# Kernel optimization log

Hardware: AMD Instinct MI355X
Metric: run time of the kernel (lower is better)

The kernel has to match this reference:

```python
import jax, jax.numpy as jnp
import numpy as np

QMAX = 127.0
EPS = 1e-08


def setup_inputs() -> dict:
    key = jax.random.key(0)
    k1, k2, k3 = jax.random.split(key, 3)
    x = jax.random.normal(k1, (4, 2048, 4096), dtype=jnp.float32)
    weight = jax.random.normal(k2, (4096, 4096), dtype=jnp.float32) * 0.02
    bias = jax.random.normal(k3, (4096,), dtype=jnp.float32) * 0.02
    return {"x": x, "weight": weight, "bias": bias}


def _quantize_weight_per_row(weight):
    # Int8WeightLinear._q_per_row: per-output-row symmetric absmax scales,
    # scale stored as fp16 (then used as fp32 at runtime).
    w = weight.astype(jnp.float32)
    s = jnp.maximum(jnp.max(jnp.abs(w), axis=1, keepdims=True), EPS) / QMAX  # [out,1]
    q = jnp.clip(jnp.round(w / s), -QMAX, QMAX).astype(jnp.int8)             # [out,in]
    s = s[:, 0].astype(jnp.float16).astype(jnp.float32)                      # [out]
    return q, s


def _quantize_activation_per_row(x2d):
    # _quantize_activation_int8_2d: per-token absmax via max(amax, -amin).
    absmax = jnp.maximum(jnp.max(x2d, axis=1), -jnp.min(x2d, axis=1))
    sc = jnp.maximum(absmax.astype(jnp.float32), EPS) / QMAX                  # [rows]
    q = jnp.clip(jnp.round(x2d.astype(jnp.float32) / sc[:, None]), -QMAX, QMAX).astype(jnp.int8)
    return q, sc


def reference(x, weight, bias):
    w_q, w_s = _quantize_weight_per_row(weight)          # int8 [out,in], fp32 [out]
    x2d = x.reshape(-1, x.shape[-1])                      # [rows, in]
    xq, x_sc = _quantize_activation_per_row(x2d)          # int8 [rows,in], fp32 [rows]
    y = jnp.matmul(xq, w_q.T, preferred_element_type=jnp.int32).astype(jnp.float32)
    y = y * x_sc[:, None] * w_s[None, :]                  # [rows, out]
    out = y.astype(x.dtype).reshape(*x.shape[:-1], weight.shape[0])
    # bias buffer is stored fp16 and cast back to activation dtype
    out = out + bias.astype(jnp.float16).astype(x.dtype)
    return out
```

## Files before the change

### kernel.cpp

```cpp
#include <hip/hip_runtime.h>
#include <hip/hip_fp16.h>

typedef int v4i __attribute__((ext_vector_type(4)));

#define QMAXF 127.0f
#define EPSF 1e-8f

template <bool WEIGHT>
__global__ __launch_bounds__(256) void quant_rows(
    const float* __restrict__ src, signed char* __restrict__ q,
    float* __restrict__ scale, int ncols) {
  const int row = blockIdx.x;
  const int t = threadIdx.x;
  const float4* s4 = (const float4*)(src + (size_t)row * ncols);

  float4 v[4];
  float am = 0.f;
#pragma unroll
  for (int p = 0; p < 4; ++p) {
    v[p] = s4[p * 256 + t];
    am = fmaxf(am, fmaxf(fmaxf(fabsf(v[p].x), fabsf(v[p].y)),
                         fmaxf(fabsf(v[p].z), fabsf(v[p].w))));
  }
#pragma unroll
  for (int off = 32; off > 0; off >>= 1) am = fmaxf(am, __shfl_xor(am, off));
  __shared__ float red[4];
  if ((t & 63) == 0) red[t >> 6] = am;
  __syncthreads();
  am = fmaxf(fmaxf(red[0], red[1]), fmaxf(red[2], red[3]));

  const float s = fmaxf(am, EPSF) / QMAXF;

  uint32_t* qrow = (uint32_t*)(q + (size_t)row * ncols);
#pragma unroll
  for (int p = 0; p < 4; ++p) {
    float fx = fminf(fmaxf(rintf(v[p].x / s), -QMAXF), QMAXF);
    float fy = fminf(fmaxf(rintf(v[p].y / s), -QMAXF), QMAXF);
    float fz = fminf(fmaxf(rintf(v[p].z / s), -QMAXF), QMAXF);
    float fw = fminf(fmaxf(rintf(v[p].w / s), -QMAXF), QMAXF);
    uint32_t packed = ((uint32_t)((int)fx & 0xff)) |
                      ((uint32_t)((int)fy & 0xff) << 8) |
                      ((uint32_t)((int)fz & 0xff) << 16) |
                      ((uint32_t)((int)fw & 0xff) << 24);
    qrow[p * 256 + t] = packed;
  }
  if (t == 0) {
    float so = s;
    if (WEIGHT) so = __half2float(__float2half(s));
    scale[row] = so;
  }
}

__device__ __forceinline__ void gload16(const void* g, void* l) {
  __builtin_amdgcn_global_load_lds(
      (const __attribute__((address_space(1))) void*)g,
      (__attribute__((address_space(3))) void*)l, 16, 0, 0);
}

#define STAGE_A(dst, br0, ktoff)                                            \
  do {                                                                      \
    gload16(Ap + (size_t)((br0) + lr) * K + (ktoff) + scsw,                 \
            (dst) + ((br0) + lr) * 128 + sc);                               \
    gload16(Ap + (size_t)((br0) + 128 + lr) * K + (ktoff) + scsw,           \
            (dst) + ((br0) + 128 + lr) * 128 + sc);                         \
  } while (0)

#define STAGE_B(dst, nh, ktoff)                                             \
  do {                                                                      \
    const int r_ = (nh)*32 + lr + (lr & 32);                                \
    gload16(Bp + (size_t)(r_) * K + (ktoff) + scsw, (dst) + r_ * 128 + sc); \
    gload16(Bp + (size_t)(r_ + 128) * K + (ktoff) + scsw,                   \
            (dst) + (r_ + 128) * 128 + sc);                                 \
  } while (0)

#define READ_AF(MH)                                                         \
  _Pragma("unroll") for (int mi = 0; mi < 4; ++mi)                          \
      _Pragma("unroll") for (int ks = 0; ks < 2; ++ks)                      \
          af[mi][ks] = *(const v4i*)(Ad + (arow + ((MH)*4 + mi) * 16) *     \
                                              128 +                        \
                                     ((ac0 + ks * 64) ^ axor))

#define READ_BF(dst, NH)                                                    \
  _Pragma("unroll") for (int ni = 0; ni < 2; ++ni)                          \
      _Pragma("unroll") for (int ks = 0; ks < 2; ++ks)                      \
          dst[ni][ks] = *(const v4i*)(Bd + (brow + ((NH)*2 + ni) * 16) *    \
                                               128 +                       \
                                      ((ac0 + ks * 64) ^ bxor))

#define MFMA_QUAD(MH, NH, BFREG)                                            \
  _Pragma("unroll") for (int ks = 0; ks < 2; ++ks)                          \
      _Pragma("unroll") for (int mi = 0; mi < 4; ++mi)                      \
          _Pragma("unroll") for (int ni = 0; ni < 2; ++ni)                  \
              acc[(MH)*4 + mi][(NH)*2 + ni] =                               \
                  __builtin_amdgcn_mfma_i32_16x16x64_i8(                    \
                      af[mi][ks], BFREG[ni][ks],                            \
                      acc[(MH)*4 + mi][(NH)*2 + ni], 0, 0, 0)

__global__ __launch_bounds__(512, 2) void gemm_i8(
    const signed char* __restrict__ A,
    const signed char* __restrict__ B,
    const float* __restrict__ xsc,
    const float* __restrict__ wsc,
    const float* __restrict__ bias,
    float* __restrict__ out, int M, int N, int K) {
  __shared__ __align__(16) signed char lds[131072];
  signed char* const ldsA = lds;
  signed char* const ldsB = lds + 65536;

  const int tid = threadIdx.x;
  const int lane = tid & 63;
  const int wid = tid >> 6;
  const int wm = wid >> 2;
  const int wn = wid & 3;
  const int bm0 = blockIdx.x * 256;
  const int bn0 = blockIdx.y * 256;

  const signed char* Ap = A + (size_t)bm0 * K;
  const signed char* Bp = B + (size_t)bn0 * K;

  const int lr = tid >> 3;
  const int sc = (tid & 7) << 4;
  const int scsw = sc ^ ((lr & 7) << 4);

  const int arow = wm * 128 + (lane & 15);
  const int brow = wn * 64 + (lane & 15);
  const int ac0 = (lane >> 4) << 4;
  const int axor = (arow & 7) << 4;
  const int bxor = (brow & 7) << 4;

  v4i acc[8][4];
#pragma unroll
  for (int i = 0; i < 8; ++i)
#pragma unroll
    for (int j = 0; j < 4; ++j) acc[i][j] = (v4i){0, 0, 0, 0};

  const int NKT = K >> 7;

  STAGE_A(ldsA, 0, 0);
  STAGE_B(ldsB, 0, 0);
  STAGE_A(ldsA, 64, 0);
  STAGE_B(ldsB, 1, 0);
  STAGE_A(ldsA + 32768, 0, 128);
  STAGE_B(ldsB + 32768, 0, 128);
  asm volatile("s_waitcnt vmcnt(4)" ::: "memory");
  __builtin_amdgcn_sched_barrier(0);
  __builtin_amdgcn_s_barrier();

  for (int kt = 0; kt < NKT; ++kt) {
    const int d = kt & 1;
    const signed char* Ad = ldsA + d * 32768;
    const signed char* Bd = ldsB + d * 32768;
    signed char* const An = ldsA + (d ^ 1) * 32768;
    signed char* const Bn = ldsB + (d ^ 1) * 32768;
    const int ko1 = (kt + 1) << 7;
    const int ko2 = (kt + 2) << 7;

    v4i af[4][2];
    v4i bf0[2][2];
    v4i bf1[2][2];

    READ_AF(0);
    READ_BF(bf0, 0);
    READ_BF(bf1, 1);
    if (kt + 1 < NKT) {
      STAGE_A(An, 64, ko1);
      STAGE_B(Bn, 1, ko1);
    }
    __builtin_amdgcn_s_setprio(1);
    MFMA_QUAD(0, 0, bf0);
    MFMA_QUAD(0, 1, bf1);
    __builtin_amdgcn_s_setprio(0);
    __builtin_amdgcn_s_barrier();

    READ_AF(1);
    if (kt + 2 < NKT) {
      STAGE_A((signed char*)Ad, 0, ko2);
      STAGE_B((signed char*)Bd, 0, ko2);
    }
    __builtin_amdgcn_s_setprio(1);
    MFMA_QUAD(1, 0, bf0);
    MFMA_QUAD(1, 1, bf1);
    __builtin_amdgcn_s_setprio(0);
    if (kt < NKT - 2) {
      asm volatile("s_waitcnt vmcnt(4)" ::: "memory");
    } else {
      asm volatile("s_waitcnt vmcnt(0)" ::: "memory");
    }
    __builtin_amdgcn_sched_barrier(0);
    __builtin_amdgcn_s_barrier();
  }

#pragma unroll
  for (int mi = 0; mi < 8; ++mi) {
    const int m0 = bm0 + wm * 128 + mi * 16 + ((lane >> 4) << 2);
    const float4 xs = *(const float4*)&xsc[m0];
    const float xsv[4] = {xs.x, xs.y, xs.z, xs.w};
#pragma unroll
    for (int ni = 0; ni < 4; ++ni) {
      const int n = bn0 + wn * 64 + ni * 16 + (lane & 15);
      const float wsn = wsc[n];
      const float bn_ = __half2float(__float2half(bias[n]));
#pragma unroll
      for (int r = 0; r < 4; ++r) {
        out[(size_t)(m0 + r) * N + n] =
            (float)acc[mi][ni][r] * xsv[r] * wsn + bn_;
      }
    }
  }
}

extern "C" void kernel_launch(void* const* d_in, const int* in_sizes, int n_in,
                              void* d_out, int out_size, void* d_ws,
                              size_t ws_size, hipStream_t stream) {
  const float* x = (const float*)d_in[0];
  const float* w = (const float*)d_in[1];
  const float* bias = (const float*)d_in[2];
  float* out = (float*)d_out;

  const int K = 4096;
  const int Nw = in_sizes[1] / K;
  const int M = in_sizes[0] / K;

  signed char* wq = (signed char*)d_ws;
  signed char* xq = wq + (size_t)Nw * K;
  float* wsc = (float*)(xq + (size_t)M * K);
  float* xsc = wsc + Nw;

  quant_rows<true><<<Nw, 256, 0, stream>>>(w, wq, wsc, K);
  quant_rows<false><<<M, 256, 0, stream>>>(x, xq, xsc, K);

  dim3 g2(M / 256, Nw / 256, 1);
  gemm_i8<<<g2, 512, 0, stream>>>(xq, wq, xsc, wsc, bias, out, M, Nw, K);
}
```

Before: 178.5 us.

## Simplify GEMM pipeline to one barrier per k-tile with k-slice MFMA ordering

Replaces the split half-tile prefetch schedule, which used two barriers per iteration and a partial vmcnt wait, with a plain double buffer. The whole next tile is staged at the top of each iteration and fully awaited at the end. The MFMA loop now iterates by k-slice (all 8x4 tiles per 64-wide slice) instead of by M/N quadrant, cutting one barrier per tile. The cost is less overlap between global loads and compute and higher register pressure from holding 8 A fragments and two sets of 4 B fragments at once.

```diff
diff --git a/kernel.cpp b/kernel.cpp
--- a/kernel.cpp
+++ b/kernel.cpp
@@ -38,11 +38,10 @@
     float fy = fminf(fmaxf(rintf(v[p].y / s), -QMAXF), QMAXF);
     float fz = fminf(fmaxf(rintf(v[p].z / s), -QMAXF), QMAXF);
     float fw = fminf(fmaxf(rintf(v[p].w / s), -QMAXF), QMAXF);
-    uint32_t packed = ((uint32_t)((int)fx & 0xff)) |
-                      ((uint32_t)((int)fy & 0xff) << 8) |
-                      ((uint32_t)((int)fz & 0xff) << 16) |
-                      ((uint32_t)((int)fw & 0xff) << 24);
-    qrow[p * 256 + t] = packed;
+    qrow[p * 256 + t] = ((uint32_t)((int)fx & 0xff)) |
+                        ((uint32_t)((int)fy & 0xff) << 8) |
+                        ((uint32_t)((int)fz & 0xff) << 16) |
+                        ((uint32_t)((int)fw & 0xff) << 24);
   }
   if (t == 0) {
     float so = s;
@@ -73,28 +72,21 @@
             (dst) + (r_ + 128) * 128 + sc);                                 \
   } while (0)
 
-#define READ_AF(MH)                                                         \
-  _Pragma("unroll") for (int mi = 0; mi < 4; ++mi)                          \
-      _Pragma("unroll") for (int ks = 0; ks < 2; ++ks)                      \
-          af[mi][ks] = *(const v4i*)(Ad + (arow + ((MH)*4 + mi) * 16) *     \
-                                              128 +                        \
-                                     ((ac0 + ks * 64) ^ axor))
-
-#define READ_BF(dst, NH)                                                    \
-  _Pragma("unroll") for (int ni = 0; ni < 2; ++ni)                          \
-      _Pragma("unroll") for (int ks = 0; ks < 2; ++ks)                      \
-          dst[ni][ks] = *(const v4i*)(Bd + (brow + ((NH)*2 + ni) * 16) *    \
-                                               128 +                       \
-                                      ((ac0 + ks * 64) ^ bxor))
-
-#define MFMA_QUAD(MH, NH, BFREG)                                            \
-  _Pragma("unroll") for (int ks = 0; ks < 2; ++ks)                          \
-      _Pragma("unroll") for (int mi = 0; mi < 4; ++mi)                      \
-          _Pragma("unroll") for (int ni = 0; ni < 2; ++ni)                  \
-              acc[(MH)*4 + mi][(NH)*2 + ni] =                               \
-                  __builtin_amdgcn_mfma_i32_16x16x64_i8(                    \
-                      af[mi][ks], BFREG[ni][ks],                            \
-                      acc[(MH)*4 + mi][(NH)*2 + ni], 0, 0, 0)
+#define READ_AF64(ks)                                                       \
+  _Pragma("unroll") for (int mi = 0; mi < 8; ++mi)                          \
+      af[mi] = *(const v4i*)(Ad + (arow + mi * 16) * 128 +                  \
+                             ((ac0 + (ks)*64) ^ axor))
+
+#define READ_BF64(dst, ks)                                                  \
+  _Pragma("unroll") for (int ni = 0; ni < 4; ++ni)                          \
+      dst[ni] = *(const v4i*)(Bd + (brow + ni * 16) * 128 +                 \
+                              ((ac0 + (ks)*64) ^ bxor))
+
+#define MFMA_SET(AF, BF)                                                    \
+  _Pragma("unroll") for (int mi = 0; mi < 8; ++mi)                          \
+      _Pragma("unroll") for (int ni = 0; ni < 4; ++ni)                      \
+          acc[mi][ni] = __builtin_amdgcn_mfma_i32_16x16x64_i8(              \
+              AF[mi], BF[ni], acc[mi][ni], 0, 0, 0)
 
 __global__ __launch_bounds__(512, 2) void gemm_i8(
     const signed char* __restrict__ A,
@@ -137,12 +129,10 @@
   const int NKT = K >> 7;
 
   STAGE_A(ldsA, 0, 0);
+  STAGE_A(ldsA, 64, 0);
   STAGE_B(ldsB, 0, 0);
-  STAGE_A(ldsA, 64, 0);
   STAGE_B(ldsB, 1, 0);
-  STAGE_A(ldsA + 32768, 0, 128);
-  STAGE_B(ldsB + 32768, 0, 128);
-  asm volatile("s_waitcnt vmcnt(4)" ::: "memory");
+  asm volatile("s_waitcnt vmcnt(0)" ::: "memory");
   __builtin_amdgcn_sched_barrier(0);
   __builtin_amdgcn_s_barrier();
 
@@ -153,39 +143,28 @@
     signed char* const An = ldsA + (d ^ 1) * 32768;
     signed char* const Bn = ldsB + (d ^ 1) * 32768;
     const int ko1 = (kt + 1) << 7;
-    const int ko2 = (kt + 2) << 7;
-
-    v4i af[4][2];
-    v4i bf0[2][2];
-    v4i bf1[2][2];
-
-    READ_AF(0);
-    READ_BF(bf0, 0);
-    READ_BF(bf1, 1);
+
+    v4i af[8];
+    v4i bf[4];
+    v4i bf2[4];
+
     if (kt + 1 < NKT) {
+      STAGE_A(An, 0, ko1);
       STAGE_A(An, 64, ko1);
+      STAGE_B(Bn, 0, ko1);
       STAGE_B(Bn, 1, ko1);
     }
+    READ_BF64(bf, 0);
+    READ_AF64(0);
+    READ_BF64(bf2, 1);
     __builtin_amdgcn_s_setprio(1);
-    MFMA_QUAD(0, 0, bf0);
-    MFMA_QUAD(0, 1, bf1);
+    MFMA_SET(af, bf);
     __builtin_amdgcn_s_setprio(0);
-    __builtin_amdgcn_s_barrier();
-
-    READ_AF(1);
-    if (kt + 2 < NKT) {
-      STAGE_A((signed char*)Ad, 0, ko2);
-      STAGE_B((signed char*)Bd, 0, ko2);
-    }
+    READ_AF64(1);
     __builtin_amdgcn_s_setprio(1);
-    MFMA_QUAD(1, 0, bf0);
-    MFMA_QUAD(1, 1, bf1);
+    MFMA_SET(af, bf2);
     __builtin_amdgcn_s_setprio(0);
-    if (kt < NKT - 2) {
-      asm volatile("s_waitcnt vmcnt(4)" ::: "memory");
-    } else {
-      asm volatile("s_waitcnt vmcnt(0)" ::: "memory");
-    }
+    asm volatile("s_waitcnt vmcnt(0)" ::: "memory");
     __builtin_amdgcn_sched_barrier(0);
     __builtin_amdgcn_s_barrier();
   }
```

New measurement: 184.8 us. 3.5% more time.

## Use 16 waves per GEMM block and merge quantization kernels

Applied to the files above, without the earlier changes.

The int8 GEMM block grows from 512 to 1024 threads over the same 256x256 tile, so each wave now owns a 64x64 sub-tile with half the accumulators, and each thread issues one async LDS load per stage instead of two. Wait counts are adjusted to match. The weight and activation quantization passes are merged into one launch to save a kernel launch. More waves can hide latency better, but launch_bounds(1024,4) cannot fit with 128KB of LDS per block and the register budget per thread becomes tight. More waves per tile also means more LDS fragment reads per MFMA.

```diff
diff --git a/kernel.cpp b/kernel.cpp
--- a/kernel.cpp
+++ b/kernel.cpp
@@ -6,11 +6,17 @@
 #define QMAXF 127.0f
 #define EPSF 1e-8f
 
-template <bool WEIGHT>
-__global__ __launch_bounds__(256) void quant_rows(
-    const float* __restrict__ src, signed char* __restrict__ q,
-    float* __restrict__ scale, int ncols) {
-  const int row = blockIdx.x;
+__global__ __launch_bounds__(256) void quant_all(
+    const float* __restrict__ w, const float* __restrict__ x,
+    signed char* __restrict__ wq, signed char* __restrict__ xq,
+    float* __restrict__ wsc, float* __restrict__ xsc, int Nw, int ncols) {
+  const int b = blockIdx.x;
+  const bool is_w = b < Nw;
+  const int row = is_w ? b : b - Nw;
+  const float* __restrict__ src = is_w ? w : x;
+  signed char* __restrict__ q = is_w ? wq : xq;
+  float* __restrict__ scale = is_w ? wsc : xsc;
+
   const int t = threadIdx.x;
   const float4* s4 = (const float4*)(src + (size_t)row * ncols);
 
@@ -38,17 +44,12 @@
     float fy = fminf(fmaxf(rintf(v[p].y / s), -QMAXF), QMAXF);
     float fz = fminf(fmaxf(rintf(v[p].z / s), -QMAXF), QMAXF);
     float fw = fminf(fmaxf(rintf(v[p].w / s), -QMAXF), QMAXF);
-    uint32_t packed = ((uint32_t)((int)fx & 0xff)) |
-                      ((uint32_t)((int)fy & 0xff) << 8) |
-                      ((uint32_t)((int)fz & 0xff) << 16) |
-                      ((uint32_t)((int)fw & 0xff) << 24);
-    qrow[p * 256 + t] = packed;
-  }
-  if (t == 0) {
-    float so = s;
-    if (WEIGHT) so = __half2float(__float2half(s));
-    scale[row] = so;
-  }
+    qrow[p * 256 + t] = ((uint32_t)((int)fx & 0xff)) |
+                        ((uint32_t)((int)fy & 0xff) << 8) |
+                        ((uint32_t)((int)fz & 0xff) << 16) |
+                        ((uint32_t)((int)fw & 0xff) << 24);
+  }
+  if (t == 0) scale[row] = is_w ? __half2float(__float2half(s)) : s;
 }
 
 __device__ __forceinline__ void gload16(const void* g, void* l) {
@@ -59,44 +60,38 @@
 
 #define STAGE_A(dst, br0, ktoff)                                            \
   do {                                                                      \
-    gload16(Ap + (size_t)((br0) + lr) * K + (ktoff) + scsw,                 \
-            (dst) + ((br0) + lr) * 128 + sc);                               \
-    gload16(Ap + (size_t)((br0) + 128 + lr) * K + (ktoff) + scsw,           \
-            (dst) + ((br0) + 128 + lr) * 128 + sc);                         \
+    const int ar_ = (br0) + (lr & 63) + ((lr >> 6) << 7);                   \
+    gload16(Ap + (size_t)ar_ * K + (ktoff) + scsw,                          \
+            (dst) + ar_ * 128 + sc);                                        \
   } while (0)
 
 #define STAGE_B(dst, nh, ktoff)                                             \
   do {                                                                      \
-    const int r_ = (nh)*32 + lr + (lr & 32);                                \
-    gload16(Bp + (size_t)(r_) * K + (ktoff) + scsw, (dst) + r_ * 128 + sc); \
-    gload16(Bp + (size_t)(r_ + 128) * K + (ktoff) + scsw,                   \
-            (dst) + (r_ + 128) * 128 + sc);                                 \
+    const int br_ = (nh)*32 + (lr & 31) + ((lr >> 5) << 6);                 \
+    gload16(Bp + (size_t)br_ * K + (ktoff) + scsw,                          \
+            (dst) + br_ * 128 + sc);                                        \
   } while (0)
 
-#define READ_AF(MH)                                                         \
-  _Pragma("unroll") for (int mi = 0; mi < 4; ++mi)                          \
+#define READ_AF(AF, MB)                                                     \
+  _Pragma("unroll") for (int mi = 0; mi < 2; ++mi)                          \
       _Pragma("unroll") for (int ks = 0; ks < 2; ++ks)                      \
-          af[mi][ks] = *(const v4i*)(Ad + (arow + ((MH)*4 + mi) * 16) *     \
-                                              128 +                        \
+          AF[mi][ks] = *(const v4i*)(Ad + (arow + ((MB) + mi) * 16) * 128 + \
                                      ((ac0 + ks * 64) ^ axor))
 
-#define READ_BF(dst, NH)                                                    \
-  _Pragma("unroll") for (int ni = 0; ni < 2; ++ni)                          \
+#define READ_BF_ALL()                                                       \
+  _Pragma("unroll") for (int ni = 0; ni < 4; ++ni)                          \
       _Pragma("unroll") for (int ks = 0; ks < 2; ++ks)                      \
-          dst[ni][ks] = *(const v4i*)(Bd + (brow + ((NH)*2 + ni) * 16) *    \
-                                               128 +                       \
-                                      ((ac0 + ks * 64) ^ bxor))
-
-#define MFMA_QUAD(MH, NH, BFREG)                                            \
+          bf[ni][ks] = *(const v4i*)(Bd + (brow + ni * 16) * 128 +          \
+                                     ((ac0 + ks * 64) ^ bxor))
+
+#define MFMA_HALF(MB, AF)                                                   \
   _Pragma("unroll") for (int ks = 0; ks < 2; ++ks)                          \
-      _Pragma("unroll") for (int mi = 0; mi < 4; ++mi)                      \
-          _Pragma("unroll") for (int ni = 0; ni < 2; ++ni)                  \
-              acc[(MH)*4 + mi][(NH)*2 + ni] =                               \
-                  __builtin_amdgcn_mfma_i32_16x16x64_i8(                    \
-                      af[mi][ks], BFREG[ni][ks],                            \
-                      acc[(MH)*4 + mi][(NH)*2 + ni], 0, 0, 0)
-
-__global__ __launch_bounds__(512, 2) void gemm_i8(
+      _Pragma("unroll") for (int mi = 0; mi < 2; ++mi)                      \
+          _Pragma("unroll") for (int ni = 0; ni < 4; ++ni)                  \
+              acc[(MB) + mi][ni] = __builtin_amdgcn_mfma_i32_16x16x64_i8(   \
+                  AF[mi][ks], bf[ni][ks], acc[(MB) + mi][ni], 0, 0, 0)
+
+__global__ __launch_bounds__(1024, 4) void gemm_i8(
     const signed char* __restrict__ A,
     const signed char* __restrict__ B,
     const float* __restrict__ xsc,
@@ -122,15 +117,15 @@
   const int sc = (tid & 7) << 4;
   const int scsw = sc ^ ((lr & 7) << 4);
 
-  const int arow = wm * 128 + (lane & 15);
+  const int arow = wm * 64 + (lane & 15);
   const int brow = wn * 64 + (lane & 15);
   const int ac0 = (lane >> 4) << 4;
   const int axor = (arow & 7) << 4;
   const int bxor = (brow & 7) << 4;
 
-  v4i acc[8][4];
-#pragma unroll
-  for (int i = 0; i < 8; ++i)
+  v4i acc[4][4];
+#pragma unroll
+  for (int i = 0; i < 4; ++i)
 #pragma unroll
     for (int j = 0; j < 4; ++j) acc[i][j] = (v4i){0, 0, 0, 0};
 
@@ -142,7 +137,7 @@
   STAGE_B(ldsB, 1, 0);
   STAGE_A(ldsA + 32768, 0, 128);
   STAGE_B(ldsB + 32768, 0, 128);
-  asm volatile("s_waitcnt vmcnt(4)" ::: "memory");
+  asm volatile("s_waitcnt vmcnt(2)" ::: "memory");
   __builtin_amdgcn_sched_barrier(0);
   __builtin_amdgcn_s_barrier();
 
@@ -155,34 +150,30 @@
     const int ko1 = (kt + 1) << 7;
     const int ko2 = (kt + 2) << 7;
 
-    v4i af[4][2];
-    v4i bf0[2][2];
-    v4i bf1[2][2];
-
-    READ_AF(0);
-    READ_BF(bf0, 0);
-    READ_BF(bf1, 1);
+    v4i af[2][2];
+    v4i bf[4][2];
+
+    READ_AF(af, 0);
+    READ_BF_ALL();
     if (kt + 1 < NKT) {
       STAGE_A(An, 64, ko1);
       STAGE_B(Bn, 1, ko1);
     }
     __builtin_amdgcn_s_setprio(1);
-    MFMA_QUAD(0, 0, bf0);
-    MFMA_QUAD(0, 1, bf1);
+    MFMA_HALF(0, af);
     __builtin_amdgcn_s_setprio(0);
     __builtin_amdgcn_s_barrier();
 
-    READ_AF(1);
+    READ_AF(af, 2);
     if (kt + 2 < NKT) {
       STAGE_A((signed char*)Ad, 0, ko2);
       STAGE_B((signed char*)Bd, 0, ko2);
     }
     __builtin_amdgcn_s_setprio(1);
-    MFMA_QUAD(1, 0, bf0);
-    MFMA_QUAD(1, 1, bf1);
+    MFMA_HALF(2, af);
     __builtin_amdgcn_s_setprio(0);
     if (kt < NKT - 2) {
-      asm volatile("s_waitcnt vmcnt(4)" ::: "memory");
+      asm volatile("s_waitcnt vmcnt(2)" ::: "memory");
     } else {
       asm volatile("s_waitcnt vmcnt(0)" ::: "memory");
     }
@@ -191,8 +182,8 @@
   }
 
 #pragma unroll
-  for (int mi = 0; mi < 8; ++mi) {
-    const int m0 = bm0 + wm * 128 + mi * 16 + ((lane >> 4) << 2);
+  for (int mi = 0; mi < 4; ++mi) {
+    const int m0 = bm0 + wm * 64 + mi * 16 + ((lane >> 4) << 2);
     const float4 xs = *(const float4*)&xsc[m0];
     const float xsv[4] = {xs.x, xs.y, xs.z, xs.w};
 #pragma unroll
@@ -226,9 +217,8 @@
   float* wsc = (float*)(xq + (size_t)M * K);
   float* xsc = wsc + Nw;
 
-  quant_rows<true><<<Nw, 256, 0, stream>>>(w, wq, wsc, K);
-  quant_rows<false><<<M, 256, 0, stream>>>(x, xq, xsc, K);
+  quant_all<<<Nw + M, 256, 0, stream>>>(w, x, wq, xq, wsc, xsc, Nw, K);
 
   dim3 g2(M / 256, Nw / 256, 1);
-  gemm_i8<<<g2, 512, 0, stream>>>(xq, wq, xsc, wsc, bias, out, M, Nw, K);
-}
+  gemm_i8<<<g2, 1024, 0, stream>>>(xq, wq, xsc, wsc, bias, out, M, Nw, K);
+}
```

Result: slower. 237.5 us (+33.0%).
